# Performance work log

Measured on AMD Instinct MI355X. Metric: run time of the kernel, lower is better.

Reference implementation:

```python
import jax, jax.numpy as jnp
import numpy as np

B, N, S = 32, 64, 9          # events, particles, particle scalars (jc, so13)
EMB, CS = 128, 32            # embedding_dim, num_channels_scalar
C2 = EMB - CS                # rank2 channels after MyLinear
NL = 4                       # Net2to2 layers
C = 128                      # working width
AVG = 49.0                   # average_nobj normalization (config 's')
METRIC = jnp.array([1.0, -1.0, -1.0, -1.0], dtype=jnp.float32)

def lrelu(x):
    return jax.nn.leaky_relu(x, 0.01)

def eq1to2(x, W, b, mask2):
    # x: [B,N,S] -> [B,N,N,CS]; 5 equivariant 1->2 basis ops, sums / AVG
    n = x.shape[1]
    eye = jnp.eye(n, dtype=x.dtype)[None, :, :, None]
    s = x.sum(1) / AVG                                   # [B,S]
    m = lambda v, k: jnp.einsum('...s,sd->...d', v, W[k])
    out = (m(x, 0)[:, :, None, :] + m(x, 1)[:, None, :, :]
           + m(x, 2)[:, :, None, :] * eye
           + m(s, 3)[:, None, None, :] + m(s, 4)[:, None, None, :] * eye)
    return lrelu(out + b) * mask2

def eq2to2(T, W, b, bd, mask2):
    # T: [B,N,N,C] (pre-masked); 15 equivariant 2->2 basis ops, sums / AVG
    n = T.shape[1]
    eye = jnp.eye(n, dtype=T.dtype)[None, :, :, None]
    d = jnp.einsum('biic->bic', T)                       # diagonal   [B,N,C]
    r = T.sum(2) / AVG                                   # row sums   [B,N,C]
    cl = T.sum(1) / AVG                                  # col sums   [B,N,C]
    t = T.sum((1, 2)) / (AVG * AVG)                      # total sum  [B,C]
    tr = d.sum(1) / AVG                                  # trace      [B,C]
    m = lambda v, k: jnp.einsum('...c,cd->...d', v, W[k])
    out = m(T, 0) + m(jnp.swapaxes(T, 1, 2), 1)
    out = out + m(d, 2)[:, :, None, :] * eye
    out = out + m(d, 3)[:, :, None, :] + m(d, 4)[:, None, :, :]
    out = out + m(r, 5)[:, :, None, :] + m(r, 6)[:, None, :, :]
    out = out + m(cl, 7)[:, :, None, :] + m(cl, 8)[:, None, :, :]
    out = out + m(r, 9)[:, :, None, :] * eye + m(cl, 10)[:, :, None, :] * eye
    out = out + m(t, 11)[:, None, None, :] + m(t, 12)[:, None, None, :] * eye
    out = out + m(tr, 13)[:, None, None, :] + m(tr, 14)[:, None, None, :] * eye
    out = out + b + bd * eye
    return lrelu(out) * mask2

def setup_inputs():
    key = jax.random.key(0)
    ks = jax.random.split(key, 32)
    p = lambda k, shape, fan: jax.random.normal(k, shape, dtype=jnp.float32) / np.float32(np.sqrt(fan))
    momenta = jax.random.normal(ks[0], (B, N, 4), dtype=jnp.float32)
    scalars = jax.random.normal(ks[1], (B, N, S), dtype=jnp.float32)
    nobj_counts = jax.random.randint(ks[2], (B,), 0, 64)
    w_lin = jnp.ones((C2, 1), jnp.float32) + 0.1 * jax.random.normal(ks[3], (C2, 1))
    alpha = jnp.ones((C2,), jnp.float32) + 0.1 * jax.random.normal(ks[4], (C2,))
    w_in = p(ks[5], (5, S, CS), 5 * S)
    b_in = jnp.zeros((CS,), jnp.float32)
    msg_w = tuple(p(ks[6 + i], (C, C), C) for i in range(NL))
    msg_b = tuple(jnp.zeros((C,), jnp.float32) for _ in range(NL))
    eq_w = tuple(p(ks[10 + i], (15, C, C), 15 * C) for i in range(NL))
    eq_b = tuple(jnp.zeros((C,), jnp.float32) for _ in range(NL))
    eq_bd = tuple(jnp.zeros((C,), jnp.float32) for _ in range(NL))
    wm0 = p(ks[20], (C, C), C)
    bm0 = jnp.zeros((C,), jnp.float32)
    w20 = p(ks[21], (2, C, C), 2 * C)
    b20 = jnp.zeros((C,), jnp.float32)
    wmlp = p(ks[22], (C, 2), C)
    bmlp = jnp.zeros((2,), jnp.float32)
    return dict(momenta=momenta, scalars=scalars, nobj_counts=nobj_counts,
                w_lin=w_lin, alpha=alpha, w_in=w_in, b_in=b_in,
                msg_w=msg_w, msg_b=msg_b, eq_w=eq_w, eq_b=eq_b, eq_bd=eq_bd,
                wm0=wm0, bm0=bm0, w20=w20, b20=b20, wmlp=wmlp, bmlp=bmlp)

def reference(momenta, scalars, nobj_counts, w_lin, alpha, w_in, b_in,
              msg_w, msg_b, eq_w, eq_b, eq_bd, wm0, bm0, w20, b20, wmlp, bmlp):
    mask1 = (jnp.arange(N)[None, :] < nobj_counts[:, None]).astype(momenta.dtype)  # [B,N]
    mask2 = (mask1[:, :, None] * mask1[:, None, :])[..., None]                     # [B,N,N,1]
    # GInvariants (so13): Minkowski dot products d_ij = p_i . p_j
    d = jnp.einsum('bic,bjc,c->bij', momenta, momenta, METRIC)[..., None]          # [B,N,N,1]
    # MyLinear: rank2_dim -> C2 channels
    r2 = jnp.einsum('bijr,cr->bijc', d, w_lin)
    # InputEncoder, 'slog' mode: per-channel scaled signed log, masked
    r2 = alpha * jnp.sign(r2) * jnp.log1p(jnp.abs(r2)) * mask2
    # Eq1to2 on particle scalars, concat with encoded rank2 invariants
    x = scalars * mask1[..., None]
    T = jnp.concatenate([eq1to2(x, w_in, b_in, mask2), r2], axis=-1)               # [B,N,N,128]
    # Net2to2: per-layer MessageNet (1x1 MLP) + Eq2to2 aggregation
    for l in range(NL):
        T = lrelu(T @ msg_w[l] + msg_b[l]) * mask2
        T = eq2to2(T, eq_w[l], eq_b[l], eq_bd[l], mask2)
    # msg_2to0 MessageNet
    T = lrelu(T @ wm0 + bm0) * mask2
    # Eq2to0: trace and total-sum invariants, activation then linear mix
    dg = jnp.einsum('biic->bc', T) / AVG
    tot = T.sum((1, 2)) / (AVG * AVG)
    agg = lrelu(jnp.stack([dg, tot], axis=1))                                      # [B,2,C]
    act3 = jnp.einsum('bkc,kcd->bd', agg, w20) + b20
    return act3 @ wmlp + bmlp                                                      # [B,2] logits
```

## Files before the change

### kernel.cpp

```cpp
#include <hip/hip_runtime.h>
#include <math.h>

#define NB 32
#define NN 64
#define NS 9
#define NCS 32
#define NC 128
#define AVGF 49.0f
#define TILE 8192

typedef __attribute__((ext_vector_type(8))) _Float16 f16x8;
typedef __attribute__((ext_vector_type(4))) _Float16 f16x4;
typedef __attribute__((ext_vector_type(4))) float f32x4;

#define MFMA(a,bb,c) c = __builtin_amdgcn_mfma_f32_16x16x32_f16(a,bb,c,0,0,0)

__device__ __forceinline__ float lrelu(float x){ return x>0.f ? x : 0.01f*x; }
__device__ __forceinline__ int tel(int j,int c){ return j*128 + (((c>>3)^(j&7))<<3) + (c&7); }

__global__ __launch_bounds__(256) void k_split(
    const float* __restrict__ m0, const float* __restrict__ m1,
    const float* __restrict__ m2, const float* __restrict__ m3,
    const float* __restrict__ m4, const float* __restrict__ e0,
    const float* __restrict__ e1, const float* __restrict__ e2,
    const float* __restrict__ e3, _Float16* __restrict__ outbuf)
{
    int m = blockIdx.y;
    const float* src;
    if (m < 5) src = (m == 0 ? m0 : m == 1 ? m1 : m == 2 ? m2 : m == 3 ? m3 : m4);
    else if (m < 13) {
        int l = (m - 5) >> 1, sub = (m - 5) & 1;
        const float* e = (l == 0 ? e0 : l == 1 ? e1 : l == 2 ? e2 : e3);
        src = e + sub * NC * NC;
    } else {
        int l = (m - 13) / 9, idx = (m - 13) % 9;
        const float* e = (l == 0 ? e0 : l == 1 ? e1 : l == 2 ? e2 : e3);
        src = e + (size_t)(2 + idx) * NC * NC;
    }
    int idx2 = blockIdx.x * 256 + threadIdx.x;
    int k = idx2 >> 7, c = idx2 & 127;
    outbuf[(size_t)m * 16384 + c * NC + k] = (_Float16)src[idx2];
}

__global__ __launch_bounds__(256) void k_prep(
    const float* __restrict__ scalars, const int* __restrict__ nobj,
    const float* __restrict__ w_in,
    float* __restrict__ mask1, float* __restrict__ P0,
    float* __restrict__ P1, float* __restrict__ P2,
    float* __restrict__ Ps3, float* __restrict__ Ps4)
{
    int b = blockIdx.x, tid = threadIdx.x;
    __shared__ float xs[NN][NS];
    __shared__ float ss[NS];
    int cnt = nobj[b];
    for (int idx = tid; idx < NN * NS; idx += 256) {
        int i = idx / NS, s = idx - i * NS;
        xs[i][s] = (i < cnt) ? scalars[(b * NN + i) * NS + s] : 0.0f;
    }
    if (tid < NN) mask1[b * NN + tid] = (tid < cnt) ? 1.0f : 0.0f;
    __syncthreads();
    if (tid < NS) {
        float a = 0.f;
        for (int i = 0; i < NN; ++i) a += xs[i][tid];
        ss[tid] = a / AVGF;
    }
    __syncthreads();
    for (int idx = tid; idx < NN * NCS; idx += 256) {
        int i = idx >> 5, d = idx & 31;
        float a0 = 0.f, a1 = 0.f, a2 = 0.f;
        #pragma unroll
        for (int s = 0; s < NS; ++s) {
            float x = xs[i][s];
            a0 += x * w_in[(0 * NS + s) * NCS + d];
            a1 += x * w_in[(1 * NS + s) * NCS + d];
            a2 += x * w_in[(2 * NS + s) * NCS + d];
        }
        P0[(b * NN + i) * NCS + d] = a0;
        P1[(b * NN + i) * NCS + d] = a1;
        P2[(b * NN + i) * NCS + d] = a2;
    }
    if (tid < NCS) {
        float a3 = 0.f, a4 = 0.f;
        #pragma unroll
        for (int s = 0; s < NS; ++s) {
            a3 += ss[s] * w_in[(3 * NS + s) * NCS + tid];
            a4 += ss[s] * w_in[(4 * NS + s) * NCS + tid];
        }
        Ps3[b * NCS + tid] = a3;
        Ps4[b * NCS + tid] = a4;
    }
}

__global__ __launch_bounds__(512, 2) void k_f0(
    const float* __restrict__ momenta, const float* __restrict__ mask1,
    const float* __restrict__ P0, const float* __restrict__ P1,
    const float* __restrict__ P2, const float* __restrict__ Ps3,
    const float* __restrict__ Ps4, const float* __restrict__ b_in,
    const float* __restrict__ w_lin, const float* __restrict__ alpha,
    const _Float16* __restrict__ Wm, const float* __restrict__ bias,
    _Float16* __restrict__ U, float* __restrict__ rsum, float* __restrict__ diag,
    float* __restrict__ pcsum)
{
    __shared__ __align__(16) char smem[44672];
    _Float16* E   = (_Float16*)smem;
    _Float16* Ust = E + TILE;
    float* mom  = (float*)(smem + 32768);
    float* P1s  = mom + 256;
    float* psb  = P1s + 2048;
    float* wl   = psb + 32;
    float* al   = wl + 96;
    float* dots = al + 96;
    float* mjv  = dots + 64;
    float* pp0  = mjv + 64;
    float* pp2  = pp0 + 32;
    float* Ls2  = pp2 + 32;
    int tid = threadIdx.x;
    int wg = blockIdx.x;
    int b = (wg & 7) * 4 + ((wg >> 3) & 3);
    int i0 = (wg >> 5) * 8;
    int chunk = wg >> 5;
    const int rb = b * NN;
    int w = tid >> 6, l = tid & 63, lr = l & 15, lk = l >> 4;
    int wr = w >> 2, wc = w & 3;
    int c0 = wc * 32 + lr, c1 = c0 + 16;
    if (tid < 64) {
        *(float4*)&mom[tid*4] = *(const float4*)&momenta[(size_t)(rb + tid) * 4];
        mjv[tid] = mask1[rb + tid];
    }
    *(float4*)&P1s[tid*4] = *(const float4*)&P1[(size_t)rb * NCS + tid*4];
    if (tid < 32) psb[tid] = Ps3[b*NCS + tid] + b_in[tid];
    if (tid >= 64 && tid < 160) { wl[tid-64] = w_lin[tid-64]; al[tid-64] = alpha[tid-64]; }
    f16x8 wmr[4][2];
    {
        const int cb = c0 * NC + lk * 8;
        #pragma unroll
        for (int kt = 0; kt < 4; ++kt)
            #pragma unroll
            for (int nt = 0; nt < 2; ++nt)
                wmr[kt][nt] = *(const f16x8*)&Wm[cb + nt*16*NC + kt*32];
    }
    float bs0 = bias[c0], bs1 = bias[c1];
    float mjc[2][4];
    #pragma unroll
    for (int mt = 0; mt < 2; ++mt)
        #pragma unroll
        for (int q = 0; q < 4; ++q)
            mjc[mt][q] = mask1[rb + (wr*2 + mt)*16 + lk*4 + q];
    float cs0[2][4], cs1[2][4];
    #pragma unroll
    for (int mt = 0; mt < 2; ++mt)
        #pragma unroll
        for (int q = 0; q < 4; ++q) { cs0[mt][q] = 0.f; cs1[mt][q] = 0.f; }

    int pj = tid >> 4, pks = tid & 15, pc0 = pks * 8;
    for (int t = 0; t < 8; ++t) {
        int i = i0 + t;
        float mi = mjv[i];
        if (tid < 64) {
            dots[tid] = mom[i*4+0]*mom[tid*4+0] - mom[i*4+1]*mom[tid*4+1]
                      - mom[i*4+2]*mom[tid*4+2] - mom[i*4+3]*mom[tid*4+3];
        } else if (tid < 96) {
            int c = tid - 64;
            pp0[c] = P0[(size_t)(rb+i)*NCS + c];
            pp2[c] = P2[(size_t)(rb+i)*NCS + c] + Ps4[b*NCS + c];
        }
        __syncthreads();
        #pragma unroll
        for (int it = 0; it < 2; ++it) {
            int j = pj + it * 32;
            float m2 = mi * mjv[j];
            float v[8];
            if (pks < 4) {
                #pragma unroll
                for (int q = 0; q < 8; ++q) {
                    float x = pp0[pc0+q] + P1s[j*NCS + pc0+q] + psb[pc0+q];
                    if (j == i) x += pp2[pc0+q];
                    v[q] = lrelu(x) * m2;
                }
            } else {
                int c2 = pc0 - NCS;
                float dj = dots[j];
                #pragma unroll
                for (int q = 0; q < 8; ++q) {
                    float r = dj * wl[c2+q];
                    float lg = __log2f(1.0f + fabsf(r));
                    float s = al[c2+q] * 0.69314718f * lg;
                    v[q] = __uint_as_float(__float_as_uint(s) ^ (__float_as_uint(r) & 0x80000000u)) * m2;
                }
            }
            f16x8 hv;
            #pragma unroll
            for (int q = 0; q < 8; ++q) hv[q] = (_Float16)v[q];
            *(f16x8*)&E[j*128 + ((pks ^ (j & 7)) * 8)] = hv;
        }
        __syncthreads();
        f32x4 acc[2][2];
        acc[0][0]=(f32x4)0.f; acc[0][1]=(f32x4)0.f; acc[1][0]=(f32x4)0.f; acc[1][1]=(f32x4)0.f;
        #pragma unroll
        for (int kt = 0; kt < 4; ++kt)
            #pragma unroll
            for (int mt = 0; mt < 2; ++mt) {
                int row = (wr*2 + mt)*16 + lr;
                int slot = ((kt*4 + lk) ^ (row & 7)) * 8;
                f16x8 a = *(const f16x8*)&E[row*128 + slot];
                #pragma unroll
                for (int nt = 0; nt < 2; ++nt)
                    MFMA(a, wmr[kt][nt], acc[mt][nt]);
            }
        float pr0 = 0.f, pr1 = 0.f;
        #pragma unroll
        for (int mt = 0; mt < 2; ++mt)
            #pragma unroll
            for (int q = 0; q < 4; ++q) {
                int j = (wr*2 + mt)*16 + lk*4 + q;
                float m2 = mi * mjc[mt][q];
                float v0 = lrelu(acc[mt][0][q] + bs0) * m2;
                float v1 = lrelu(acc[mt][1][q] + bs1) * m2;
                pr0 += v0; pr1 += v1;
                cs0[mt][q] += v0; cs1[mt][q] += v1;
                if (j == i) {
                    diag[(size_t)(rb+i)*NC + c0] = v0;
                    diag[(size_t)(rb+i)*NC + c1] = v1;
                }
                Ust[tel(j, c0)] = (_Float16)v0;
                Ust[tel(j, c1)] = (_Float16)v1;
            }
        pr0 += __shfl_xor(pr0, 16); pr0 += __shfl_xor(pr0, 32);
        pr1 += __shfl_xor(pr1, 16); pr1 += __shfl_xor(pr1, 32);
        if (l < 16) { Ls2[wr*128 + c0] = pr0; Ls2[wr*128 + c1] = pr1; }
        __syncthreads();
        size_t t0 = (size_t)(rb + i) * TILE;
        *(f16x8*)&U[t0 + (size_t)tid*8] = *(const f16x8*)&Ust[tid*8];
        *(f16x8*)&U[t0 + (size_t)(tid+512)*8] = *(const f16x8*)&Ust[(tid+512)*8];
        if (tid < 128)
            rsum[(size_t)(rb+i)*NC + tid] = (Ls2[tid] + Ls2[128 + tid]) / AVGF;
    }
    const size_t RN = (size_t)NB * NN * NC;
    #pragma unroll
    for (int mt = 0; mt < 2; ++mt)
        #pragma unroll
        for (int q = 0; q < 4; ++q) {
            int j = (wr*2 + mt)*16 + lk*4 + q;
            pcsum[(size_t)chunk * RN + (size_t)(rb+j)*NC + c0] = cs0[mt][q];
            pcsum[(size_t)chunk * RN + (size_t)(rb+j)*NC + c1] = cs1[mt][q];
        }
}

template<int WOUT>
__global__ __launch_bounds__(512, 2) void k_feq(
    const _Float16* __restrict__ Uin,
    const _Float16* __restrict__ W0, const _Float16* __restrict__ W1,
    const _Float16* __restrict__ Wm, const float* __restrict__ mbias,
    const float* __restrict__ A, const float* __restrict__ Bc,
    const float* __restrict__ Dgv, const float* __restrict__ G,
    const float* __restrict__ Gd, const float* __restrict__ mask1,
    _Float16* __restrict__ Uo, float* __restrict__ rsum, float* __restrict__ diag,
    float* __restrict__ pcsum)
{
    __shared__ __align__(16) char smem[66560];
    _Float16* PA  = (_Float16*)smem;
    _Float16* PB  = (_Float16*)(smem + 16384);
    _Float16* E   = (_Float16*)(smem + 32768);
    _Float16* Ust = (_Float16*)(smem + 49152);
    float* Ls2    = (float*)(smem + 65536);
    int tid = threadIdx.x;
    int wg = blockIdx.x;
    int b = (wg & 7) * 4 + ((wg >> 3) & 3);
    int i0 = (wg >> 5) * 8;
    int chunk = wg >> 5;
    const int rb = b * NN;
    int w = tid >> 6, l = tid & 63, lr = l & 15, lk = l >> 4;
    int wr = w >> 2, wc = w & 3;
    int c0 = wc * 32 + lr, c1 = c0 + 16;

    f16x8 w0r[4][2], w1r[4][2], wmr[4][2];
    {
        const int cb = c0 * NC + lk * 8;
        #pragma unroll
        for (int kt = 0; kt < 4; ++kt)
            #pragma unroll
            for (int nt = 0; nt < 2; ++nt) {
                w0r[kt][nt] = *(const f16x8*)&W0[cb + nt*16*NC + kt*32];
                w1r[kt][nt] = *(const f16x8*)&W1[cb + nt*16*NC + kt*32];
                wmr[kt][nt] = *(const f16x8*)&Wm[cb + nt*16*NC + kt*32];
            }
    }
    float G0 = G[(size_t)b*NC + c0], G1 = G[(size_t)b*NC + c1];
    float Gd0 = Gd[(size_t)b*NC + c0], Gd1 = Gd[(size_t)b*NC + c1];
    float mb0 = mbias[c0], mb1 = mbias[c1];
    float Bv0[2][4], Bv1[2][4], mjc[2][4], cs0[2][4], cs1[2][4];
    #pragma unroll
    for (int mt = 0; mt < 2; ++mt)
        #pragma unroll
        for (int q = 0; q < 4; ++q) {
            int j = (wr*2 + mt)*16 + lk*4 + q;
            Bv0[mt][q] = Bc[(size_t)(rb+j)*NC + c0];
            Bv1[mt][q] = Bc[(size_t)(rb+j)*NC + c1];
            mjc[mt][q] = mask1[rb + j];
            cs0[mt][q] = 0.f; cs1[mt][q] = 0.f;
        }

    int sj = tid >> 4, sks = tid & 15;
    {
        size_t t0 = (size_t)(rb + i0) * TILE;
        int isw = i0 & 7;
        f16x8 r0 = *(const f16x8*)&Uin[t0 + (size_t)tid*8];
        f16x8 r1 = *(const f16x8*)&Uin[t0 + (size_t)(tid+512)*8];
        f16x8 r2 = *(const f16x8*)&Uin[(size_t)(rb+sj)*TILE + i0*128 + ((sks^isw)*8)];
        f16x8 r3 = *(const f16x8*)&Uin[(size_t)(rb+sj+32)*TILE + i0*128 + ((sks^isw)*8)];
        *(f16x8*)&PA[tid*8] = r0;
        *(f16x8*)&PA[(tid+512)*8] = r1;
        *(f16x8*)&PB[sj*128 + ((sks^(sj&7))*8)] = r2;
        *(f16x8*)&PB[(sj+32)*128 + ((sks^((sj+32)&7))*8)] = r3;
    }
    __syncthreads();

    for (int t = 0; t < 8; ++t) {
        int i = i0 + t;
        float mi = mask1[rb + i];
        float A0v = A[(size_t)(rb+i)*NC + c0] + G0;
        float A1v = A[(size_t)(rb+i)*NC + c1] + G1;
        float D0v = Dgv[(size_t)(rb+i)*NC + c0] + Gd0;
        float D1v = Dgv[(size_t)(rb+i)*NC + c1] + Gd1;
        f16x8 r0, r1, r2, r3;
        if (t < 7) {
            int in_ = i + 1;
            size_t t0n = (size_t)(rb + in_) * TILE;
            int isw = in_ & 7;
            r0 = *(const f16x8*)&Uin[t0n + (size_t)tid*8];
            r1 = *(const f16x8*)&Uin[t0n + (size_t)(tid+512)*8];
            r2 = *(const f16x8*)&Uin[(size_t)(rb+sj)*TILE + in_*128 + ((sks^isw)*8)];
            r3 = *(const f16x8*)&Uin[(size_t)(rb+sj+32)*TILE + in_*128 + ((sks^isw)*8)];
        }
        f32x4 acc[2][2];
        acc[0][0]=(f32x4)0.f; acc[0][1]=(f32x4)0.f; acc[1][0]=(f32x4)0.f; acc[1][1]=(f32x4)0.f;
        #pragma unroll
        for (int kt = 0; kt < 4; ++kt)
            #pragma unroll
            for (int mt = 0; mt < 2; ++mt) {
                int row = (wr*2 + mt)*16 + lr;
                int slot = ((kt*4 + lk) ^ (row & 7)) * 8;
                f16x8 a1 = *(const f16x8*)&PA[row*128 + slot];
                f16x8 a2 = *(const f16x8*)&PB[row*128 + slot];
                #pragma unroll
                for (int nt = 0; nt < 2; ++nt) {
                    MFMA(a1, w0r[kt][nt], acc[mt][nt]);
                    MFMA(a2, w1r[kt][nt], acc[mt][nt]);
                }
            }
        float m2v[2][4];
        #pragma unroll
        for (int mt = 0; mt < 2; ++mt)
            #pragma unroll
            for (int q = 0; q < 4; ++q) {
                int j = (wr*2 + mt)*16 + lk*4 + q;
                float m2 = mi * mjc[mt][q];
                m2v[mt][q] = m2;
                float v0 = acc[mt][0][q] + A0v + Bv0[mt][q];
                float v1 = acc[mt][1][q] + A1v + Bv1[mt][q];
                if (j == i) { v0 += D0v; v1 += D1v; }
                v0 = lrelu(v0) * m2;
                v1 = lrelu(v1) * m2;
                E[tel(j, c0)] = (_Float16)v0;
                E[tel(j, c1)] = (_Float16)v1;
            }
        __syncthreads();
        if (t < 7) {
            int in_ = i + 1;
            *(f16x8*)&PA[tid*8] = r0;
            *(f16x8*)&PA[(tid+512)*8] = r1;
            *(f16x8*)&PB[sj*128 + ((sks^(sj&7))*8)] = r2;
            *(f16x8*)&PB[(sj+32)*128 + ((sks^((sj+32)&7))*8)] = r3;
            (void)in_;
        }
        acc[0][0]=(f32x4)0.f; acc[0][1]=(f32x4)0.f; acc[1][0]=(f32x4)0.f; acc[1][1]=(f32x4)0.f;
        #pragma unroll
        for (int kt = 0; kt < 4; ++kt)
            #pragma unroll
            for (int mt = 0; mt < 2; ++mt) {
                int row = (wr*2 + mt)*16 + lr;
                int slot = ((kt*4 + lk) ^ (row & 7)) * 8;
                f16x8 e = *(const f16x8*)&E[row*128 + slot];
                #pragma unroll
                for (int nt = 0; nt < 2; ++nt)
                    MFMA(e, wmr[kt][nt], acc[mt][nt]);
            }
        float pr0 = 0.f, pr1 = 0.f;
        #pragma unroll
        for (int mt = 0; mt < 2; ++mt)
            #pragma unroll
            for (int q = 0; q < 4; ++q) {
                int j = (wr*2 + mt)*16 + lk*4 + q;
                float v0 = lrelu(acc[mt][0][q] + mb0) * m2v[mt][q];
                float v1 = lrelu(acc[mt][1][q] + mb1) * m2v[mt][q];
                pr0 += v0; pr1 += v1;
                if (WOUT) { cs0[mt][q] += v0; cs1[mt][q] += v1; }
                if (j == i) {
                    diag[(size_t)(rb+i)*NC + c0] = v0;
                    diag[(size_t)(rb+i)*NC + c1] = v1;
                }
                if (WOUT) {
                    Ust[tel(j, c0)] = (_Float16)v0;
                    Ust[tel(j, c1)] = (_Float16)v1;
                }
            }
        pr0 += __shfl_xor(pr0, 16); pr0 += __shfl_xor(pr0, 32);
        pr1 += __shfl_xor(pr1, 16); pr1 += __shfl_xor(pr1, 32);
        if (l < 16) { Ls2[wr*128 + c0] = pr0; Ls2[wr*128 + c1] = pr1; }
        __syncthreads();
        if (WOUT) {
            size_t t0 = (size_t)(rb + i) * TILE;
            *(f16x8*)&Uo[t0 + (size_t)tid*8] = *(const f16x8*)&Ust[tid*8];
            *(f16x8*)&Uo[t0 + (size_t)(tid+512)*8] = *(const f16x8*)&Ust[(tid+512)*8];
        }
        if (tid < 128)
            rsum[(size_t)(rb+i)*NC + tid] = (Ls2[tid] + Ls2[128 + tid]) / AVGF;
    }
    if (WOUT) {
        const size_t RN = (size_t)NB * NN * NC;
        #pragma unroll
        for (int mt = 0; mt < 2; ++mt)
            #pragma unroll
            for (int q = 0; q < 4; ++q) {
                int j = (wr*2 + mt)*16 + lk*4 + q;
                pcsum[(size_t)chunk * RN + (size_t)(rb+j)*NC + c0] = cs0[mt][q];
                pcsum[(size_t)chunk * RN + (size_t)(rb+j)*NC + c1] = cs1[mt][q];
            }
    }
}

__global__ __launch_bounds__(512, 2) void k_red3(
    const float* __restrict__ rsum, const float* __restrict__ pcsum,
    const float* __restrict__ diag, const _Float16* __restrict__ Wt,
    const float* __restrict__ Weq, const float* __restrict__ eqb,
    const float* __restrict__ eqbd,
    float* __restrict__ A, float* __restrict__ Bc, float* __restrict__ Dgv,
    float* __restrict__ G, float* __restrict__ Gd)
{
    __shared__ __align__(16) char smem[50176];
    _Float16* Pd = (_Float16*)smem;
    _Float16* Pr = Pd + 2048;
    _Float16* Pc = Pr + 2048;
    _Float16* WL = Pc + 2048;
    float* tsp  = (float*)(smem + 45056);
    float* trsp = tsp + 512;
    float* ts   = trsp + 512;
    float* trs  = ts + 128;
    int tid = threadIdx.x;
    int wg = blockIdx.x;
    int b = (wg & 7) * 4 + ((wg >> 3) & 3);
    int quarter = wg >> 5;
    int row0 = quarter * 16;
    const int rb = b * NN;
    const size_t RN = (size_t)NB * NN * NC;
    int w = tid >> 6, l = tid & 63, lr = l & 15, lk = l >> 4;
    int col = w * 16 + lr;

    {
        int s = tid & 255, prow = s >> 4, pks = s & 15;
        const float* src = (tid < 256 ? diag : rsum) + (size_t)(rb + row0 + prow) * NC + pks * 8;
        float4 f0 = *(const float4*)src, f1 = *(const float4*)(src + 4);
        float vv[8] = {f0.x,f0.y,f0.z,f0.w,f1.x,f1.y,f1.z,f1.w};
        f16x8 hv;
        #pragma unroll
        for (int q = 0; q < 8; ++q) hv[q] = (_Float16)vv[q];
        _Float16* dst = (tid < 256 ? Pd : Pr);
        *(f16x8*)&dst[prow*128 + ((pks ^ (prow & 7)) * 8)] = hv;
    }
    {
        int prow = tid >> 5, kq = tid & 31;
        size_t o = (size_t)(rb + row0 + prow) * NC + kq * 4;
        float s0 = 0, s1 = 0, s2 = 0, s3 = 0;
        #pragma unroll
        for (int ch = 0; ch < 8; ++ch) {
            float4 v = *(const float4*)&pcsum[(size_t)ch * RN + o];
            s0 += v.x; s1 += v.y; s2 += v.z; s3 += v.w;
        }
        f16x4 hv;
        hv[0] = (_Float16)(s0 / AVGF); hv[1] = (_Float16)(s1 / AVGF);
        hv[2] = (_Float16)(s2 / AVGF); hv[3] = (_Float16)(s3 / AVGF);
        *(f16x4*)&Pc[prow*128 + (((kq >> 1) ^ (prow & 7)) << 3) + (kq & 1) * 4] = hv;
    }
    if (quarter == 0) {
        int c = tid & 127, part = tid >> 7;
        float st = 0.f, sd = 0.f;
        for (int ii = part*16; ii < part*16 + 16; ++ii) {
            st += rsum[(size_t)(rb+ii)*NC + c];
            sd += diag[(size_t)(rb+ii)*NC + c];
        }
        tsp[part*128 + c] = st;
        trsp[part*128 + c] = sd;
    }
    f16x8 wreg[4];
    #pragma unroll
    for (int it = 0; it < 4; ++it) {
        int s = tid + it*512, c = s >> 4, ks = s & 15;
        wreg[it] = *(const f16x8*)&Wt[c*128 + ks*8];
    }
    __syncthreads();
    #pragma unroll
    for (int it = 0; it < 4; ++it) {
        int s = tid + it*512, c = s >> 4, ks = s & 15;
        *(f16x8*)&WL[c*128 + ((ks ^ (c & 7)) * 8)] = wreg[it];
    }
    if (quarter == 0 && tid < 256) {
        int c = tid & 127;
        float* dst = (tid < 128 ? ts : trs);
        float* src = (tid < 128 ? tsp : trsp);
        dst[c] = (src[c] + src[128+c] + src[256+c] + src[384+c]) / AVGF;
    }

    f32x4 acc3[3];
    acc3[0] = (f32x4)0.f; acc3[1] = (f32x4)0.f; acc3[2] = (f32x4)0.f;
    const int pan[9] = {0,0,0,1,1,2,2,1,2};
    const int outp[9] = {2,0,1,0,1,0,1,2,2};
    #pragma unroll
    for (int m = 0; m < 9; ++m) {
        __syncthreads();
        if (m < 8) {
            const _Float16* Wn = Wt + (size_t)(m+1) * 16384;
            #pragma unroll
            for (int it = 0; it < 4; ++it) {
                int s = tid + it*512, c = s >> 4, ks = s & 15;
                wreg[it] = *(const f16x8*)&Wn[c*128 + ks*8];
            }
        }
        const _Float16* P = (pan[m] == 0 ? Pd : pan[m] == 1 ? Pr : Pc);
        #pragma unroll
        for (int kt = 0; kt < 4; ++kt) {
            f16x8 a = *(const f16x8*)&P[lr*128 + (((kt*4+lk) ^ (lr & 7)) * 8)];
            f16x8 bb = *(const f16x8*)&WL[col*128 + (((kt*4+lk) ^ (lr & 7)) * 8)];
            MFMA(a, bb, acc3[outp[m]]);
        }
        __syncthreads();
        if (m < 8) {
            #pragma unroll
            for (int it = 0; it < 4; ++it) {
                int s = tid + it*512, c = s >> 4, ks = s & 15;
                *(f16x8*)&WL[c*128 + ((ks ^ (c & 7)) * 8)] = wreg[it];
            }
        }
    }
    #pragma unroll
    for (int q = 0; q < 4; ++q) {
        size_t o = (size_t)(rb + row0 + lk*4 + q) * NC + col;
        A[o]   = acc3[0][q];
        Bc[o]  = acc3[1][q];
        Dgv[o] = acc3[2][q];
    }
    if (quarter == 0) {
        __syncthreads();
        int c = tid & 127, part = tid >> 7;
        float g = 0.f, gd = 0.f;
        for (int k = part*32; k < part*32 + 32; ++k) {
            float tv = ts[k], rv = trs[k];
            g  += tv * Weq[(11*NC + k)*NC + c] + rv * Weq[(13*NC + k)*NC + c];
            gd += tv * Weq[(12*NC + k)*NC + c] + rv * Weq[(14*NC + k)*NC + c];
        }
        tsp[part*128 + c] = g;
        trsp[part*128 + c] = gd;
        __syncthreads();
        if (tid < 128) {
            float gg = eqb[tid] + tsp[tid] + tsp[128+tid] + tsp[256+tid] + tsp[384+tid];
            float gdd = eqbd[tid] + trsp[tid] + trsp[128+tid] + trsp[256+tid] + trsp[384+tid];
            G[b*NC + tid] = gg;
            Gd[b*NC + tid] = gdd;
        }
    }
}

__global__ __launch_bounds__(128) void k_final(
    const float* __restrict__ rsum, const float* __restrict__ diag,
    const float* __restrict__ w20, const float* __restrict__ b20,
    const float* __restrict__ wmlp, const float* __restrict__ bmlp,
    float* __restrict__ outp)
{
    int b = blockIdx.x;
    int c = threadIdx.x;
    __shared__ float agg0[NC], agg1[NC], act3[NC];
    float dgv = 0.f, tot = 0.f;
    for (int i = 0; i < NN; ++i) {
        dgv += diag[(size_t)(b * NN + i) * NC + c];
        tot += rsum[(size_t)(b * NN + i) * NC + c];
    }
    agg0[c] = lrelu(dgv / AVGF);
    agg1[c] = lrelu(tot / AVGF);
    __syncthreads();
    float a3 = b20[c];
    for (int k = 0; k < NC; ++k)
        a3 += agg0[k] * w20[k * NC + c] + agg1[k] * w20[(NC + k) * NC + c];
    act3[c] = a3;
    __syncthreads();
    if (c < 2) {
        float o = bmlp[c];
        for (int d = 0; d < NC; ++d) o += act3[d] * wmlp[d * 2 + c];
        outp[b * 2 + c] = o;
    }
}

extern "C" void kernel_launch(void* const* d_in, const int* in_sizes, int n_in,
                              void* d_out, int out_size, void* d_ws, size_t ws_size,
                              hipStream_t stream)
{
    const float* momenta = (const float*)d_in[0];
    const float* scalars = (const float*)d_in[1];
    const int*   nobj    = (const int*)d_in[2];
    const float* w_lin   = (const float*)d_in[3];
    const float* alpha   = (const float*)d_in[4];
    const float* w_in    = (const float*)d_in[5];
    const float* b_in    = (const float*)d_in[6];
    const float *msgW[4], *msgB[4], *eqW[4], *eqB[4], *eqBd[4];
    const float *wm0, *bm0, *w20, *b20, *wmlp, *bmlp;
    if (n_in >= 33) {
        for (int l = 0; l < 4; ++l) {
            msgW[l] = (const float*)d_in[7 + l];
            msgB[l] = (const float*)d_in[11 + l];
            eqW[l]  = (const float*)d_in[15 + l];
            eqB[l]  = (const float*)d_in[19 + l];
            eqBd[l] = (const float*)d_in[23 + l];
        }
        wm0  = (const float*)d_in[27]; bm0  = (const float*)d_in[28];
        w20  = (const float*)d_in[29]; b20  = (const float*)d_in[30];
        wmlp = (const float*)d_in[31]; bmlp = (const float*)d_in[32];
    } else {
        for (int l = 0; l < 4; ++l) {
            msgW[l] = (const float*)d_in[7] + (size_t)l * NC * NC;
            msgB[l] = (const float*)d_in[8] + l * NC;
            eqW[l]  = (const float*)d_in[9] + (size_t)l * 15 * NC * NC;
            eqB[l]  = (const float*)d_in[10] + l * NC;
            eqBd[l] = (const float*)d_in[11] + l * NC;
        }
        wm0  = (const float*)d_in[12]; bm0  = (const float*)d_in[13];
        w20  = (const float*)d_in[14]; b20  = (const float*)d_in[15];
        wmlp = (const float*)d_in[16]; bmlp = (const float*)d_in[17];
    }

    const size_t TN2 = (size_t)NB * NN * TILE;
    const size_t RN  = (size_t)NB * NN * NC;
    _Float16* X  = (_Float16*)d_ws;
    _Float16* Y  = X + TN2;
    _Float16* SW = Y + TN2;
    float* fp = (float*)(((uintptr_t)(SW + 49 * 16384) + 15) & ~(uintptr_t)15);
    float* rsum  = fp;
    float* pcsum = rsum + RN;
    float* diag  = pcsum + 8 * RN;
    float* Aa    = diag + RN;
    float* Bb    = Aa + RN;
    float* Dgv   = Bb + RN;
    float* G     = Dgv + RN;
    float* Gd    = G + NB * NC;
    float* mask1 = Gd + NB * NC;
    float* P0    = mask1 + NB * NN;
    float* P1    = P0 + (size_t)NB * NN * NCS;
    float* P2    = P1 + (size_t)NB * NN * NCS;
    float* Ps3   = P2 + (size_t)NB * NN * NCS;
    float* Ps4   = Ps3 + NB * NCS;
    size_t need = (size_t)((char*)(Ps4 + NB * NCS) - (char*)d_ws);
    if (ws_size < need) return;

    k_split<<<dim3(64, 49), 256, 0, stream>>>(msgW[0], msgW[1], msgW[2], msgW[3],
                                              wm0, eqW[0], eqW[1], eqW[2], eqW[3], SW);
    k_prep<<<NB, 256, 0, stream>>>(scalars, nobj, w_in, mask1, P0, P1, P2, Ps3, Ps4);

    k_f0<<<256, 512, 0, stream>>>(momenta, mask1, P0, P1, P2, Ps3, Ps4,
                                  b_in, w_lin, alpha, SW ,
                                  msgB[0], X, rsum, diag, pcsum);

    _Float16 *in = X, *out = Y;
    for (int l = 0; l < 4; ++l) {
        _Float16* Wt = SW + (size_t)(13 + l * 9) * 16384;
        k_red3<<<128, 512, 0, stream>>>(rsum, pcsum, diag, Wt, eqW[l],
                                        eqB[l], eqBd[l], Aa, Bb, Dgv, G, Gd);
        _Float16* W0 = SW + (size_t)(5 + 2 * l) * 16384;
        _Float16* W1 = W0 + 16384;
        if (l < 3) {
            _Float16* Wm = SW + (size_t)(l + 1) * 16384;
            k_feq<1><<<256, 512, 0, stream>>>(in, W0, W1, Wm, msgB[l + 1],
                                              Aa, Bb, Dgv, G, Gd, mask1,
                                              out, rsum, diag, pcsum);
            _Float16* t = in; in = out; out = t;
        } else {
            _Float16* Wm = SW + (size_t)4 * 16384;
            k_feq<0><<<256, 512, 0, stream>>>(in, W0, W1, Wm, bm0,
                                              Aa, Bb, Dgv, G, Gd, mask1,
                                              out, rsum, diag, pcsum);
        }
    }
    k_final<<<NB, 128, 0, stream>>>(rsum, diag, w20, b20, wmlp, bmlp, (float*)d_out);
}
```

Measured before the change: 233.5 us.

## Use 1024-thread blocks in k_feq with one M-tile per wave, Wm staged in LDS

Doubles the k_feq workgroup to 16 waves so each wave handles one 16-row slice instead of two, halving per-thread accumulators and per-thread global loads. The message-weight matrix Wm moves from registers into a swizzled 32KB LDS buffer to cut register pressure. The row-sum reduction now combines four partial rows. The aim is more latency hiding per CU, at the cost of extra LDS reads per MFMA, a larger LDS footprint, and a launch bound (1024,4) that LDS size cannot actually meet.

```diff
diff --git a/kernel.cpp b/kernel.cpp
--- a/kernel.cpp
+++ b/kernel.cpp
@@ -247,7 +247,7 @@
 }
 
 template<int WOUT>
-__global__ __launch_bounds__(512, 2) void k_feq(
+__global__ __launch_bounds__(1024, 4) void k_feq(
     const _Float16* __restrict__ Uin,
     const _Float16* __restrict__ W0, const _Float16* __restrict__ W1,
     const _Float16* __restrict__ Wm, const float* __restrict__ mbias,
@@ -257,61 +257,58 @@
     _Float16* __restrict__ Uo, float* __restrict__ rsum, float* __restrict__ diag,
     float* __restrict__ pcsum)
 {
-    __shared__ __align__(16) char smem[66560];
+    __shared__ __align__(16) char smem[100352];
     _Float16* PA  = (_Float16*)smem;
     _Float16* PB  = (_Float16*)(smem + 16384);
     _Float16* E   = (_Float16*)(smem + 32768);
     _Float16* Ust = (_Float16*)(smem + 49152);
-    float* Ls2    = (float*)(smem + 65536);
+    _Float16* WmL = (_Float16*)(smem + 65536);
+    float* Ls2    = (float*)(smem + 98304);
     int tid = threadIdx.x;
     int wg = blockIdx.x;
     int b = (wg & 7) * 4 + ((wg >> 3) & 3);
-    int i0 = (wg >> 5) * 8;
     int chunk = wg >> 5;
+    int i0 = chunk * 8;
     const int rb = b * NN;
     int w = tid >> 6, l = tid & 63, lr = l & 15, lk = l >> 4;
     int wr = w >> 2, wc = w & 3;
     int c0 = wc * 32 + lr, c1 = c0 + 16;
-
-    f16x8 w0r[4][2], w1r[4][2], wmr[4][2];
-    {
-        const int cb = c0 * NC + lk * 8;
-        #pragma unroll
-        for (int kt = 0; kt < 4; ++kt)
-            #pragma unroll
-            for (int nt = 0; nt < 2; ++nt) {
-                w0r[kt][nt] = *(const f16x8*)&W0[cb + nt*16*NC + kt*32];
-                w1r[kt][nt] = *(const f16x8*)&W1[cb + nt*16*NC + kt*32];
-                wmr[kt][nt] = *(const f16x8*)&Wm[cb + nt*16*NC + kt*32];
-            }
+    const int cb = c0 * NC + lk * 8;
+
+    f16x8 w0r[4][2], w1r[4][2];
+    #pragma unroll
+    for (int kt = 0; kt < 4; ++kt)
+        #pragma unroll
+        for (int nt = 0; nt < 2; ++nt) {
+            w0r[kt][nt] = *(const f16x8*)&W0[cb + nt*16*NC + kt*32];
+            w1r[kt][nt] = *(const f16x8*)&W1[cb + nt*16*NC + kt*32];
+        }
+    #pragma unroll
+    for (int it = 0; it < 2; ++it) {
+        int s = tid + it * 1024, c = s >> 4, ks = s & 15;
+        *(f16x8*)&WmL[c*128 + ((ks ^ (c & 7)) * 8)] = *(const f16x8*)&Wm[c*128 + ks*8];
     }
     float G0 = G[(size_t)b*NC + c0], G1 = G[(size_t)b*NC + c1];
     float Gd0 = Gd[(size_t)b*NC + c0], Gd1 = Gd[(size_t)b*NC + c1];
     float mb0 = mbias[c0], mb1 = mbias[c1];
-    float Bv0[2][4], Bv1[2][4], mjc[2][4], cs0[2][4], cs1[2][4];
-    #pragma unroll
-    for (int mt = 0; mt < 2; ++mt)
-        #pragma unroll
-        for (int q = 0; q < 4; ++q) {
-            int j = (wr*2 + mt)*16 + lk*4 + q;
-            Bv0[mt][q] = Bc[(size_t)(rb+j)*NC + c0];
-            Bv1[mt][q] = Bc[(size_t)(rb+j)*NC + c1];
-            mjc[mt][q] = mask1[rb + j];
-            cs0[mt][q] = 0.f; cs1[mt][q] = 0.f;
-        }
+    float Bv0[4], Bv1[4], mjc[4], cs0[4], cs1[4];
+    #pragma unroll
+    for (int q = 0; q < 4; ++q) {
+        int j = wr*16 + lk*4 + q;
+        Bv0[q] = Bc[(size_t)(rb+j)*NC + c0];
+        Bv1[q] = Bc[(size_t)(rb+j)*NC + c1];
+        mjc[q] = mask1[rb + j];
+        cs0[q] = 0.f; cs1[q] = 0.f;
+    }
 
     int sj = tid >> 4, sks = tid & 15;
     {
         size_t t0 = (size_t)(rb + i0) * TILE;
         int isw = i0 & 7;
         f16x8 r0 = *(const f16x8*)&Uin[t0 + (size_t)tid*8];
-        f16x8 r1 = *(const f16x8*)&Uin[t0 + (size_t)(tid+512)*8];
-        f16x8 r2 = *(const f16x8*)&Uin[(size_t)(rb+sj)*TILE + i0*128 + ((sks^isw)*8)];
-        f16x8 r3 = *(const f16x8*)&Uin[(size_t)(rb+sj+32)*TILE + i0*128 + ((sks^isw)*8)];
+        f16x8 r1 = *(const f16x8*)&Uin[(size_t)(rb+sj)*TILE + i0*128 + ((sks^isw)*8)];
         *(f16x8*)&PA[tid*8] = r0;
-        *(f16x8*)&PA[(tid+512)*8] = r1;
-        *(f16x8*)&PB[sj*128 + ((sks^(sj&7))*8)] = r2;
-        *(f16x8*)&PB[(sj+32)*128 + ((sks^((sj+32)&7))*8)] = r3;
+        *(f16x8*)&PB[sj*128 + ((sks^(sj&7))*8)] = r1;
     }
     __syncthreads();
 
@@ -322,88 +319,77 @@
         float A1v = A[(size_t)(rb+i)*NC + c1] + G1;
         float D0v = Dgv[(size_t)(rb+i)*NC + c0] + Gd0;
         float D1v = Dgv[(size_t)(rb+i)*NC + c1] + Gd1;
-        f16x8 r0, r1, r2, r3;
+        f16x8 r0, r1;
         if (t < 7) {
             int in_ = i + 1;
             size_t t0n = (size_t)(rb + in_) * TILE;
             int isw = in_ & 7;
             r0 = *(const f16x8*)&Uin[t0n + (size_t)tid*8];
-            r1 = *(const f16x8*)&Uin[t0n + (size_t)(tid+512)*8];
-            r2 = *(const f16x8*)&Uin[(size_t)(rb+sj)*TILE + in_*128 + ((sks^isw)*8)];
-            r3 = *(const f16x8*)&Uin[(size_t)(rb+sj+32)*TILE + in_*128 + ((sks^isw)*8)];
-        }
-        f32x4 acc[2][2];
-        acc[0][0]=(f32x4)0.f; acc[0][1]=(f32x4)0.f; acc[1][0]=(f32x4)0.f; acc[1][1]=(f32x4)0.f;
-        #pragma unroll
-        for (int kt = 0; kt < 4; ++kt)
-            #pragma unroll
-            for (int mt = 0; mt < 2; ++mt) {
-                int row = (wr*2 + mt)*16 + lr;
-                int slot = ((kt*4 + lk) ^ (row & 7)) * 8;
-                f16x8 a1 = *(const f16x8*)&PA[row*128 + slot];
-                f16x8 a2 = *(const f16x8*)&PB[row*128 + slot];
-                #pragma unroll
-                for (int nt = 0; nt < 2; ++nt) {
-                    MFMA(a1, w0r[kt][nt], acc[mt][nt]);
-                    MFMA(a2, w1r[kt][nt], acc[mt][nt]);
-                }
-            }
-        float m2v[2][4];
-        #pragma unroll
-        for (int mt = 0; mt < 2; ++mt)
-            #pragma unroll
-            for (int q = 0; q < 4; ++q) {
-                int j = (wr*2 + mt)*16 + lk*4 + q;
-                float m2 = mi * mjc[mt][q];
-                m2v[mt][q] = m2;
-                float v0 = acc[mt][0][q] + A0v + Bv0[mt][q];
-                float v1 = acc[mt][1][q] + A1v + Bv1[mt][q];
-                if (j == i) { v0 += D0v; v1 += D1v; }
-                v0 = lrelu(v0) * m2;
-                v1 = lrelu(v1) * m2;
-                E[tel(j, c0)] = (_Float16)v0;
-                E[tel(j, c1)] = (_Float16)v1;
-            }
+            r1 = *(const f16x8*)&Uin[(size_t)(rb+sj)*TILE + in_*128 + ((sks^isw)*8)];
+        }
+        f32x4 acc[2];
+        acc[0] = (f32x4)0.f; acc[1] = (f32x4)0.f;
+        #pragma unroll
+        for (int kt = 0; kt < 4; ++kt) {
+            int row = wr*16 + lr;
+            int slot = ((kt*4 + lk) ^ (row & 7)) * 8;
+            f16x8 a1 = *(const f16x8*)&PA[row*128 + slot];
+            f16x8 a2 = *(const f16x8*)&PB[row*128 + slot];
+            #pragma unroll
+            for (int nt = 0; nt < 2; ++nt) {
+                MFMA(a1, w0r[kt][nt], acc[nt]);
+                MFMA(a2, w1r[kt][nt], acc[nt]);
+            }
+        }
+        float m2v[4];
+        #pragma unroll
+        for (int q = 0; q < 4; ++q) {
+            int j = wr*16 + lk*4 + q;
+            float m2 = mi * mjc[q];
+            m2v[q] = m2;
+            float v0 = acc[0][q] + A0v + Bv0[q];
+            float v1 = acc[1][q] + A1v + Bv1[q];
+            if (j == i) { v0 += D0v; v1 += D1v; }
+            v0 = lrelu(v0) * m2;
+            v1 = lrelu(v1) * m2;
+            E[tel(j, c0)] = (_Float16)v0;
+            E[tel(j, c1)] = (_Float16)v1;
+        }
         __syncthreads();
         if (t < 7) {
-            int in_ = i + 1;
             *(f16x8*)&PA[tid*8] = r0;
-            *(f16x8*)&PA[(tid+512)*8] = r1;
-            *(f16x8*)&PB[sj*128 + ((sks^(sj&7))*8)] = r2;
-            *(f16x8*)&PB[(sj+32)*128 + ((sks^((sj+32)&7))*8)] = r3;
-            (void)in_;
-        }
-        acc[0][0]=(f32x4)0.f; acc[0][1]=(f32x4)0.f; acc[1][0]=(f32x4)0.f; acc[1][1]=(f32x4)0.f;
-        #pragma unroll
-        for (int kt = 0; kt < 4; ++kt)
-            #pragma unroll
-            for (int mt = 0; mt < 2; ++mt) {
-                int row = (wr*2 + mt)*16 + lr;
-                int slot = ((kt*4 + lk) ^ (row & 7)) * 8;
-                f16x8 e = *(const f16x8*)&E[row*128 + slot];
-                #pragma unroll
-                for (int nt = 0; nt < 2; ++nt)
-                    MFMA(e, wmr[kt][nt], acc[mt][nt]);
-            }
+            *(f16x8*)&PB[sj*128 + ((sks^(sj&7))*8)] = r1;
+        }
+        acc[0] = (f32x4)0.f; acc[1] = (f32x4)0.f;
+        #pragma unroll
+        for (int kt = 0; kt < 4; ++kt) {
+            int row = wr*16 + lr;
+            int slot = ((kt*4 + lk) ^ (row & 7)) * 8;
+            f16x8 e = *(const f16x8*)&E[row*128 + slot];
+            #pragma unroll
+            for (int nt = 0; nt < 2; ++nt) {
+                int cw = wc*32 + nt*16 + lr;
+                f16x8 bh = *(const f16x8*)&WmL[cw*128 + (((kt*4 + lk) ^ (lr & 7)) * 8)];
+                MFMA(e, bh, acc[nt]);
+            }
+        }
         float pr0 = 0.f, pr1 = 0.f;
         #pragma unroll
-        for (int mt = 0; mt < 2; ++mt)
-            #pragma unroll
-            for (int q = 0; q < 4; ++q) {
-                int j = (wr*2 + mt)*16 + lk*4 + q;
-                float v0 = lrelu(acc[mt][0][q] + mb0) * m2v[mt][q];
-                float v1 = lrelu(acc[mt][1][q] + mb1) * m2v[mt][q];
-                pr0 += v0; pr1 += v1;
-                if (WOUT) { cs0[mt][q] += v0; cs1[mt][q] += v1; }
-                if (j == i) {
-                    diag[(size_t)(rb+i)*NC + c0] = v0;
-                    diag[(size_t)(rb+i)*NC + c1] = v1;
-                }
-                if (WOUT) {
-                    Ust[tel(j, c0)] = (_Float16)v0;
-                    Ust[tel(j, c1)] = (_Float16)v1;
-                }
-            }
+        for (int q = 0; q < 4; ++q) {
+            int j = wr*16 + lk*4 + q;
+            float v0 = lrelu(acc[0][q] + mb0) * m2v[q];
+            float v1 = lrelu(acc[1][q] + mb1) * m2v[q];
+            pr0 += v0; pr1 += v1;
+            if (WOUT) { cs0[q] += v0; cs1[q] += v1; }
+            if (j == i) {
+                diag[(size_t)(rb+i)*NC + c0] = v0;
+                diag[(size_t)(rb+i)*NC + c1] = v1;
+            }
+            if (WOUT) {
+                Ust[tel(j, c0)] = (_Float16)v0;
+                Ust[tel(j, c1)] = (_Float16)v1;
+            }
+        }
         pr0 += __shfl_xor(pr0, 16); pr0 += __shfl_xor(pr0, 32);
         pr1 += __shfl_xor(pr1, 16); pr1 += __shfl_xor(pr1, 32);
         if (l < 16) { Ls2[wr*128 + c0] = pr0; Ls2[wr*128 + c1] = pr1; }
@@ -411,21 +397,19 @@
         if (WOUT) {
             size_t t0 = (size_t)(rb + i) * TILE;
             *(f16x8*)&Uo[t0 + (size_t)tid*8] = *(const f16x8*)&Ust[tid*8];
-            *(f16x8*)&Uo[t0 + (size_t)(tid+512)*8] = *(const f16x8*)&Ust[(tid+512)*8];
         }
         if (tid < 128)
-            rsum[(size_t)(rb+i)*NC + tid] = (Ls2[tid] + Ls2[128 + tid]) / AVGF;
+            rsum[(size_t)(rb+i)*NC + tid] =
+                (Ls2[tid] + Ls2[128+tid] + Ls2[256+tid] + Ls2[384+tid]) / AVGF;
     }
     if (WOUT) {
         const size_t RN = (size_t)NB * NN * NC;
         #pragma unroll
-        for (int mt = 0; mt < 2; ++mt)
-            #pragma unroll
-            for (int q = 0; q < 4; ++q) {
-                int j = (wr*2 + mt)*16 + lk*4 + q;
-                pcsum[(size_t)chunk * RN + (size_t)(rb+j)*NC + c0] = cs0[mt][q];
-                pcsum[(size_t)chunk * RN + (size_t)(rb+j)*NC + c1] = cs1[mt][q];
-            }
+        for (int q = 0; q < 4; ++q) {
+            int j = wr*16 + lk*4 + q;
+            pcsum[(size_t)chunk * RN + (size_t)(rb+j)*NC + c0] = cs0[q];
+            pcsum[(size_t)chunk * RN + (size_t)(rb+j)*NC + c1] = cs1[q];
+        }
     }
 }
 
@@ -675,15 +659,15 @@
         _Float16* W1 = W0 + 16384;
         if (l < 3) {
             _Float16* Wm = SW + (size_t)(l + 1) * 16384;
-            k_feq<1><<<256, 512, 0, stream>>>(in, W0, W1, Wm, msgB[l + 1],
-                                              Aa, Bb, Dgv, G, Gd, mask1,
-                                              out, rsum, diag, pcsum);
+            k_feq<1><<<256, 1024, 0, stream>>>(in, W0, W1, Wm, msgB[l + 1],
+                                               Aa, Bb, Dgv, G, Gd, mask1,
+                                               out, rsum, diag, pcsum);
             _Float16* t = in; in = out; out = t;
         } else {
             _Float16* Wm = SW + (size_t)4 * 16384;
-            k_feq<0><<<256, 512, 0, stream>>>(in, W0, W1, Wm, bm0,
-                                              Aa, Bb, Dgv, G, Gd, mask1,
-                                              out, rsum, diag, pcsum);
+            k_feq<0><<<256, 1024, 0, stream>>>(in, W0, W1, Wm, bm0,
+                                               Aa, Bb, Dgv, G, Gd, mask1,
+                                               out, rsum, diag, pcsum);
         }
     }
     k_final<<<NB, 128, 0, stream>>>(rsum, diag, w20, b20, wmlp, bmlp, (float*)d_out);
```

Measured after the change: 450.6 us. 92.9% more time.
